# Kernel tuning notes

Measured on AMD Instinct MI355X. Metric: run time of the kernel, lower is better.

## Reference

```python
import jax, jax.numpy as jnp
import numpy as np

HIDDEN = 1024
N_HEADS = 16
HEAD_DIM = HIDDEN // N_HEADS


def setup_inputs() -> dict:
    key = jax.random.key(0)
    ks = jax.random.split(key, 9)
    s = 1.0 / np.sqrt(HIDDEN)
    d = {"hidden_states": jax.random.normal(ks[0], (2, 2048, HIDDEN), dtype=jnp.float32)}
    for i, name in enumerate(["q", "k", "v", "o"]):
        d[f"W{name}"] = jax.random.uniform(ks[1 + 2 * i], (HIDDEN, HIDDEN), minval=-s, maxval=s, dtype=jnp.float32)
        d[f"b{name}"] = jax.random.uniform(ks[2 + 2 * i], (HIDDEN,), minval=-s, maxval=s, dtype=jnp.float32)
    return d


def reference(hidden_states, Wq, bq, Wk, bk, Wv, bv, Wo, bo):
    B, L, _ = hidden_states.shape

    def shape(x):  # (B, L, H*D) -> (B, H, L, D)
        return x.reshape(B, L, N_HEADS, HEAD_DIM).transpose(0, 2, 1, 3)

    q = shape(hidden_states @ Wq.T + bq)
    k = shape(hidden_states @ Wk.T + bk)
    v = shape(hidden_states @ Wv.T + bv)
    scores = jnp.einsum("bhqd,bhkd->bhqk", q, k) / jnp.sqrt(jnp.float32(HEAD_DIM))
    attn = jax.nn.softmax(scores, axis=-1)
    ctx = jnp.einsum("bhqk,bhkd->bhqd", attn, v)
    ctx = ctx.transpose(0, 2, 1, 3).reshape(B, L, HIDDEN)
    return ctx @ Wo.T + bo
```

## Files before the change

### kernel.cpp

```cpp
#include <hip/hip_runtime.h>
#include <hip/hip_bf16.h>
#include <stdint.h>

typedef __bf16 bf16_t;
typedef __bf16 bf16x8 __attribute__((ext_vector_type(8)));
typedef __bf16 bf16x4 __attribute__((ext_vector_type(4)));
typedef float  f32x4  __attribute__((ext_vector_type(4)));
typedef float  f32x16 __attribute__((ext_vector_type(16)));

__device__ __forceinline__ f32x4 mfma16(bf16x8 a, bf16x8 b, f32x4 c) {
    return __builtin_amdgcn_mfma_f32_16x16x32_bf16(a, b, c, 0, 0, 0);
}
__device__ __forceinline__ f32x16 mfma32(bf16x8 a, bf16x8 b, f32x16 c) {
    return __builtin_amdgcn_mfma_f32_32x32x16_bf16(a, b, c, 0, 0, 0);
}
__device__ __forceinline__ void gload16(const void* g, void* l) {
    __builtin_amdgcn_global_load_lds(
        (const __attribute__((address_space(1))) unsigned int*)g,
        (__attribute__((address_space(3))) unsigned int*)l, 16, 0, 0);
}
__device__ __forceinline__ unsigned cvtpk(float lo, float hi_) {
    unsigned r;
    asm("v_cvt_pk_bf16_f32 %0, %1, %2" : "=v"(r) : "v"(lo), "v"(hi_));
    return r;
}
__device__ __forceinline__ float fexp2(float x) {
    return __builtin_amdgcn_exp2f(x);
}

__global__ __launch_bounds__(256) void split_all(const float* __restrict__ X,
                                                 const float* __restrict__ w0, const float* __restrict__ w1,
                                                 const float* __restrict__ w2, const float* __restrict__ w3,
                                                 bf16_t* __restrict__ xh,
                                                 bf16_t* __restrict__ h0, bf16_t* __restrict__ h1,
                                                 bf16_t* __restrict__ h2, bf16_t* __restrict__ h3) {
    int blk = blockIdx.x;
    const float* in;
    bf16_t* hi;
    int i;
    if (blk < 2048) {
        in = X; hi = xh;
        i = blk * 256 + threadIdx.x;
    } else {
        int s = (blk - 2048) >> 9;
        in = (s == 0) ? w0 : (s == 1) ? w1 : (s == 2) ? w2 : w3;
        hi = (s == 0) ? h0 : (s == 1) ? h1 : (s == 2) ? h2 : h3;
        i = ((blk - 2048) & 511) * 256 + threadIdx.x;
    }
    int row = i >> 7;
    int di = (i & ~3) | ((i & 3) ^ ((row >> 1) & 3));
    const float4* in4 = reinterpret_cast<const float4*>(in);
    float4 v0 = in4[2 * i], v1 = in4[2 * i + 1];
    float vv[8] = {v0.x, v0.y, v0.z, v0.w, v1.x, v1.y, v1.z, v1.w};
    bf16x8 h;
#pragma unroll
    for (int j = 0; j < 8; ++j) h[j] = (bf16_t)vv[j];
    reinterpret_cast<bf16x8*>(hi)[di] = h;
}

__global__ __launch_bounds__(512) void gemm_qkv(const bf16_t* __restrict__ Xhi,
                                                const bf16_t* __restrict__ Wqh,
                                                const bf16_t* __restrict__ Wkh,
                                                const bf16_t* __restrict__ Wvh,
                                                const float* __restrict__ bq, const float* __restrict__ bk,
                                                const float* __restrict__ bv,
                                                bf16_t* __restrict__ Qb, bf16_t* __restrict__ Kb,
                                                bf16_t* __restrict__ Vt) {
    __shared__ alignas(16) bf16_t ldsA[2][128 * 32];
    __shared__ alignas(16) bf16_t ldsB[2][128 * 32];
    const int tid = threadIdx.x, wave = tid >> 6, lane = tid & 63;
    const int g = lane >> 4, cc = lane & 15;
    const int bx = blockIdx.x, which = bx >> 3;
    const bf16_t* Bh = (which == 0) ? Wqh : (which == 1) ? Wkh : Wvh;
    const float* bias = (which == 0) ? bq : (which == 1) ? bk : bv;
    const float scale = (which == 0) ? 0.125f * 1.4426950408889634f : 1.0f;
    const int mBase = blockIdx.y * 128, nB = (bx & 7) * 128;
    const int wm = wave >> 2, wn = wave & 3;

    f32x4 zero = {0.f, 0.f, 0.f, 0.f};
    f32x4 acc[4][2];
#pragma unroll
    for (int mi = 0; mi < 4; ++mi)
#pragma unroll
        for (int ni = 0; ni < 2; ++ni) acc[mi][ni] = zero;

    auto stage = [&](int k0, int buf) {
#pragma unroll
        for (int i = 0; i < 2; ++i) {
            int c = wave + 8 * i;
            int tile = c >> 3, sub = c & 7;
            int row = sub * 16 + (lane >> 2);
            int colE = (lane & 3) * 8;
            const bf16_t* src = (tile == 0) ? Xhi + (size_t)(mBase + row) * 1024 + k0 + colE
                                            : Bh + (size_t)(nB + row) * 1024 + k0 + colE;
            bf16_t* dst = (tile == 0) ? ldsA[buf] : ldsB[buf];
            gload16(src, (char*)dst + sub * 1024);
        }
    };

    stage(0, 0);
    for (int t = 0; t < 32; ++t) {
        const int buf = t & 1;
        asm volatile("s_waitcnt vmcnt(0)" ::: "memory");
        __builtin_amdgcn_s_barrier();
        __builtin_amdgcn_sched_barrier(0);
        if (t < 31) stage((t + 1) * 32, buf ^ 1);
        {
            bf16x8 af[4], bf_[2];
#pragma unroll
            for (int mi = 0; mi < 4; ++mi) {
                int ra = wm * 64 + mi * 16 + cc;
                af[mi] = *reinterpret_cast<const bf16x8*>(
                    (const char*)ldsA[buf] + ra * 64 + ((g ^ ((ra >> 1) & 3)) * 16));
            }
#pragma unroll
            for (int ni = 0; ni < 2; ++ni) {
                int rb = wn * 32 + ni * 16 + cc;
                bf_[ni] = *reinterpret_cast<const bf16x8*>(
                    (const char*)ldsB[buf] + rb * 64 + ((g ^ ((rb >> 1) & 3)) * 16));
            }
#pragma unroll
            for (int mi = 0; mi < 4; ++mi)
#pragma unroll
                for (int ni = 0; ni < 2; ++ni)
                    acc[mi][ni] = mfma16(af[mi], bf_[ni], acc[mi][ni]);
        }
    }

#pragma unroll
    for (int mi = 0; mi < 4; ++mi)
#pragma unroll
        for (int ni = 0; ni < 2; ++ni)
#pragma unroll
            for (int r = 0; r < 4; ++r) {
                int row = mBase + wm * 64 + mi * 16 + g * 4 + r;
                int colL = nB + wn * 32 + ni * 16 + cc;
                float v = (acc[mi][ni][r] + bias[colL]) * scale;
                int b = row >> 11, tok = row & 2047, h = colL >> 6, d = colL & 63;
                if (which == 2) {
                    int kt = tok >> 6, key = tok & 63;
                    size_t o = (((size_t)(b * 16 + h) * 32 + kt) * 4096)
                             + d * 64 + ((((key >> 3) ^ (d & 7)) << 3) | (key & 7));
                    Vt[o] = (bf16_t)v;
                } else {
                    int dd = (which == 1) ? ((((d >> 3) ^ (tok & 7)) << 3) | (d & 7)) : d;
                    bf16_t* out = (which == 0) ? Qb : Kb;
                    out[((size_t)(b * 16 + h) * 2048 + tok) * 64 + dd] = (bf16_t)v;
                }
            }
}

__global__ __launch_bounds__(512) void gemm_o(const bf16_t* __restrict__ Ahi,
                                              const bf16_t* __restrict__ Bhi,
                                              const float* __restrict__ bias,
                                              float* __restrict__ outF) {
    __shared__ alignas(16) bf16_t ldsA[2][64 * 32];
    __shared__ alignas(16) bf16_t ldsB[2][128 * 32];
    const int tid = threadIdx.x, wave = tid >> 6, lane = tid & 63;
    const int g = lane >> 4, cc = lane & 15;
    const int mBase = blockIdx.y * 64, nBase = blockIdx.x * 128;
    const int wm = wave >> 2, wn = wave & 3;

    f32x4 zero = {0.f, 0.f, 0.f, 0.f};
    f32x4 acc[2][2];
#pragma unroll
    for (int mi = 0; mi < 2; ++mi)
#pragma unroll
        for (int ni = 0; ni < 2; ++ni) acc[mi][ni] = zero;

    auto stage = [&](int k0, int buf) {
#pragma unroll
        for (int i = 0; i < 2; ++i) {
            int c = wave + 8 * i;
            if (c >= 12) continue;
            const bf16_t* srcb;
            bf16_t* dst;
            int sub, rbase;
            if (c < 4) { srcb = Ahi; dst = ldsA[buf]; sub = c;     rbase = mBase; }
            else       { srcb = Bhi; dst = ldsB[buf]; sub = c - 4; rbase = nBase; }
            int row = sub * 16 + (lane >> 2);
            int colE = (lane & 3) * 8;
            gload16(srcb + (size_t)(rbase + row) * 1024 + k0 + colE, (char*)dst + sub * 1024);
        }
    };

    stage(0, 0);
    for (int t = 0; t < 32; ++t) {
        const int buf = t & 1;
        asm volatile("s_waitcnt vmcnt(0)" ::: "memory");
        __builtin_amdgcn_s_barrier();
        __builtin_amdgcn_sched_barrier(0);
        if (t < 31) stage((t + 1) * 32, buf ^ 1);
        {
            bf16x8 af[2], bf_[2];
#pragma unroll
            for (int mi = 0; mi < 2; ++mi) {
                int ra = wm * 32 + mi * 16 + cc;
                af[mi] = *reinterpret_cast<const bf16x8*>(
                    (const char*)ldsA[buf] + ra * 64 + ((g ^ ((ra >> 1) & 3)) * 16));
            }
#pragma unroll
            for (int ni = 0; ni < 2; ++ni) {
                int rb = wn * 32 + ni * 16 + cc;
                bf_[ni] = *reinterpret_cast<const bf16x8*>(
                    (const char*)ldsB[buf] + rb * 64 + ((g ^ ((rb >> 1) & 3)) * 16));
            }
#pragma unroll
            for (int mi = 0; mi < 2; ++mi)
#pragma unroll
                for (int ni = 0; ni < 2; ++ni)
                    acc[mi][ni] = mfma16(af[mi], bf_[ni], acc[mi][ni]);
        }
    }

#pragma unroll
    for (int mi = 0; mi < 2; ++mi)
#pragma unroll
        for (int ni = 0; ni < 2; ++ni)
#pragma unroll
            for (int r = 0; r < 4; ++r) {
                int row = mBase + wm * 32 + mi * 16 + g * 4 + r;
                int col = nBase + wn * 32 + ni * 16 + cc;
                outF[(size_t)row * 1024 + col] = acc[mi][ni][r] + bias[col];
            }
}

__global__ __launch_bounds__(512, 4) void attn_kernel(const bf16_t* __restrict__ Qb,
                                                      const bf16_t* __restrict__ Kb_p,
                                                      const bf16_t* __restrict__ Vt_p,
                                                      bf16_t* __restrict__ ctxHi) {
    __shared__ alignas(16) bf16_t SB[2][16384];

    const int lid = blockIdx.x;
    const int xcd = lid & 7, slot = lid >> 3;
    const int bh = xcd * 4 + (slot & 3);
    const int qt = slot >> 2;

    const int tid = threadIdx.x, w = tid >> 6, l = tid & 63;
    const int ql = l & 31, hi = l >> 5;
    const int wq = w & 3;
    const int par = w >> 2;
    const size_t kbase = (size_t)bh * 2048 * 64;
    const unsigned rsw = (unsigned)(ql & 7) << 4;

    bf16x8 qf[4];
    {
        const bf16_t* qp = Qb + kbase + (size_t)(qt * 128 + wq * 32 + ql) * 64 + hi * 8;
#pragma unroll
        for (int c = 0; c < 4; ++c) qf[c] = *reinterpret_cast<const bf16x8*>(qp + c * 16);
    }
    bf16x8 ones;
#pragma unroll
    for (int j = 0; j < 8; ++j) ones[j] = (bf16_t)1.0f;

    f32x16 O0{}, O1{}, Lacc{};

    auto stage = [&](int r) {
        int buf = r & 1;
        const bf16_t* ks = Kb_p + kbase + (size_t)(2 * r) * 4096;
        const bf16_t* vs = Vt_p + ((size_t)bh * 32 + 2 * r) * 4096;
        char* kd = (char*)&SB[buf][0];
        char* vd = (char*)&SB[buf][8192];
        gload16(ks + (size_t)tid * 8,        kd + tid * 16);
        gload16(ks + (size_t)tid * 8 + 4096, kd + tid * 16 + 8192);
        gload16(vs + (size_t)tid * 8,        vd + tid * 16);
        gload16(vs + (size_t)tid * 8 + 4096, vd + tid * 16 + 8192);
    };

    stage(0);

    for (int r = 0; r < 16; ++r) {
        const int buf = r & 1;
        asm volatile("s_waitcnt vmcnt(0)" ::: "memory");
        __builtin_amdgcn_s_barrier();
        __builtin_amdgcn_sched_barrier(0);
        if (r < 15) stage(r + 1);

        const char* kb = (const char*)&SB[buf][par * 4096];
        const char* vb = (const char*)&SB[buf][8192 + par * 4096];

        f32x16 S0{}, S1{};
        __builtin_amdgcn_s_setprio(1);
#pragma unroll
        for (int c = 0; c < 4; ++c) {
            unsigned col = ((unsigned)(c * 32 + hi * 16)) ^ rsw;
            bf16x8 k0 = *reinterpret_cast<const bf16x8*>(kb + (unsigned)ql * 128 + col);
            bf16x8 k1 = *reinterpret_cast<const bf16x8*>(kb + (unsigned)(32 + ql) * 128 + col);
            S0 = mfma32(k0, qf[c], S0);
            S1 = mfma32(k1, qf[c], S1);
        }
        __builtin_amdgcn_s_setprio(0);

#pragma unroll
        for (int r2 = 0; r2 < 16; ++r2) {
            S0[r2] = fexp2(S0[r2]);
            S1[r2] = fexp2(S1[r2]);
        }

        union U { unsigned u[4]; bf16x8 v; };
        bf16x8 PB[4];
#define MKFRAG(DST, SS, M8)                                                       \
        {                                                                         \
            unsigned c0 = cvtpk(SS[M8 + 0], SS[M8 + 1]);                          \
            unsigned c1 = cvtpk(SS[M8 + 2], SS[M8 + 3]);                          \
            unsigned c2 = cvtpk(SS[M8 + 4], SS[M8 + 5]);                          \
            unsigned c3 = cvtpk(SS[M8 + 6], SS[M8 + 7]);                          \
            unsigned y0 = hi ? c0 : c2;                                           \
            unsigned y1 = hi ? c1 : c3;                                           \
            unsigned z0 = (unsigned)__shfl_xor((int)y0, 32);                      \
            unsigned z1 = (unsigned)__shfl_xor((int)y1, 32);                      \
            U uu;                                                                 \
            uu.u[0] = hi ? z0 : c0;                                               \
            uu.u[1] = hi ? z1 : c1;                                               \
            uu.u[2] = hi ? c2 : z0;                                               \
            uu.u[3] = hi ? c3 : z1;                                               \
            DST = uu.v;                                                           \
        }
        MKFRAG(PB[0], S0, 0)
        MKFRAG(PB[1], S0, 8)
        MKFRAG(PB[2], S1, 0)
        MKFRAG(PB[3], S1, 8)
#undef MKFRAG

        __builtin_amdgcn_s_setprio(1);
#pragma unroll
        for (int ks = 0; ks < 4; ++ks) {
            unsigned col = ((unsigned)(ks * 32 + hi * 16)) ^ rsw;
            bf16x8 v0 = *reinterpret_cast<const bf16x8*>(vb + (unsigned)ql * 128 + col);
            bf16x8 v1 = *reinterpret_cast<const bf16x8*>(vb + (unsigned)(32 + ql) * 128 + col);
            O0 = mfma32(v0, PB[ks], O0);
            O1 = mfma32(v1, PB[ks], O1);
            Lacc = mfma32(ones, PB[ks], Lacc);
        }
        __builtin_amdgcn_s_setprio(0);
    }

    __builtin_amdgcn_s_barrier();

    float lsum = Lacc[0];
    float* mbuf = (float*)&SB[0][0];
    if (par == 1) {
        float* p = mbuf + (size_t)(wq * 64 + l) * 33;
        p[0] = lsum;
#pragma unroll
        for (int r2 = 0; r2 < 16; ++r2) { p[1 + r2] = O0[r2]; p[17 + r2] = O1[r2]; }
    }
    __syncthreads();
    if (par == 1) return;

    {
        const float* p = mbuf + (size_t)(wq * 64 + l) * 33;
        lsum += p[0];
#pragma unroll
        for (int r2 = 0; r2 < 16; ++r2) {
            O0[r2] += p[1 + r2];
            O1[r2] += p[17 + r2];
        }
    }

    const int b = bh >> 4, h = bh & 15;
    const int ltok = qt * 128 + wq * 32 + ql;
    const float inv = 1.0f / lsum;
    bf16_t* baseH = ctxHi + ((size_t)(b * 2048 + ltok)) * 1024 + h * 64;
    const int rsw4 = (ql >> 1) & 3;
#define WRITE4(OT, RQ, DT)                                                      \
    {                                                                           \
        int d0 = (RQ ^ rsw4) * 8 + 4 * hi + 32 * DT;                            \
        bf16x4 vh;                                                              \
        _Pragma("unroll")                                                       \
        for (int i = 0; i < 4; ++i) {                                           \
            float v = OT[4 * RQ + i] * inv;                                     \
            vh[i] = (bf16_t)v;                                                  \
        }                                                                       \
        *reinterpret_cast<bf16x4*>(baseH + d0) = vh;                            \
    }
    WRITE4(O0, 0, 0) WRITE4(O0, 1, 0) WRITE4(O0, 2, 0) WRITE4(O0, 3, 0)
    WRITE4(O1, 0, 1) WRITE4(O1, 1, 1) WRITE4(O1, 2, 1) WRITE4(O1, 3, 1)
#undef WRITE4
}

extern "C" void kernel_launch(void* const* d_in, const int* in_sizes, int n_in,
                              void* d_out, int out_size, void* d_ws, size_t ws_size,
                              hipStream_t stream) {
    const float* X  = (const float*)d_in[0];
    const float* Wq = (const float*)d_in[1];
    const float* bq = (const float*)d_in[2];
    const float* Wk = (const float*)d_in[3];
    const float* bk = (const float*)d_in[4];
    const float* Wv = (const float*)d_in[5];
    const float* bv = (const float*)d_in[6];
    const float* Wo = (const float*)d_in[7];
    const float* bo = (const float*)d_in[8];

    const size_t MB = 1024 * 1024;
    char* ws = (char*)d_ws;
    bf16_t* Xhi = (bf16_t*)(ws);
    bf16_t* Wqh = (bf16_t*)(ws + 8 * MB);
    bf16_t* Wkh = (bf16_t*)(ws + 10 * MB);
    bf16_t* Wvh = (bf16_t*)(ws + 12 * MB);
    bf16_t* Woh = (bf16_t*)(ws + 14 * MB);
    bf16_t* Qb  = (bf16_t*)(ws + 24 * MB);
    bf16_t* Kb  = (bf16_t*)(ws + 32 * MB);
    bf16_t* Vt  = (bf16_t*)(ws + 40 * MB);
    bf16_t* Chi = (bf16_t*)(ws + 48 * MB);

    split_all<<<4096, 256, 0, stream>>>(X, Wq, Wk, Wv, Wo,
                                        Xhi, Wqh, Wkh, Wvh, Woh);

    dim3 qkvGrid(24, 32);
    gemm_qkv<<<qkvGrid, 512, 0, stream>>>(Xhi, Wqh, Wkh, Wvh,
                                          bq, bk, bv, Qb, Kb, Vt);

    attn_kernel<<<512, 512, 0, stream>>>(Qb, Kb, Vt, Chi);

    dim3 oGrid(8, 64);
    gemm_o<<<oGrid, 512, 0, stream>>>(Chi, Woh, bo, (float*)d_out);
}
```

Baseline: 112.4 us.

## Triple-buffer GEMM loads and drop key-split reduction in attention

Both GEMMs move from double to triple-buffered LDS staging with a partial vmcnt wait, so the load for tile t+2 is in flight while tile t is computed. The output GEMM goes to 256 threads, with each wave covering all 64 rows and a 32-column slice. The attention kernel drops its two-way key split across wave groups and the LDS reduction at the end; it now runs 256 threads per block that walk all 32 key tiles, with occupancy hint 5. This removes the reduction and a barrier but halves the per-block parallelism and doubles the serial key loop.

```diff
diff --git a/kernel.cpp b/kernel.cpp
--- a/kernel.cpp
+++ b/kernel.cpp
@@ -66,8 +66,8 @@
                                                 const float* __restrict__ bv,
                                                 bf16_t* __restrict__ Qb, bf16_t* __restrict__ Kb,
                                                 bf16_t* __restrict__ Vt) {
-    __shared__ alignas(16) bf16_t ldsA[2][128 * 32];
-    __shared__ alignas(16) bf16_t ldsB[2][128 * 32];
+    __shared__ alignas(16) bf16_t ldsA[3][128 * 32];
+    __shared__ alignas(16) bf16_t ldsB[3][128 * 32];
     const int tid = threadIdx.x, wave = tid >> 6, lane = tid & 63;
     const int g = lane >> 4, cc = lane & 15;
     const int bx = blockIdx.x, which = bx >> 3;
@@ -99,25 +99,30 @@
     };
 
     stage(0, 0);
+    stage(32, 1);
+    int cur = 0;
     for (int t = 0; t < 32; ++t) {
-        const int buf = t & 1;
-        asm volatile("s_waitcnt vmcnt(0)" ::: "memory");
+        if (t < 31) asm volatile("s_waitcnt vmcnt(2)" ::: "memory");
+        else        asm volatile("s_waitcnt vmcnt(0)" ::: "memory");
         __builtin_amdgcn_s_barrier();
         __builtin_amdgcn_sched_barrier(0);
-        if (t < 31) stage((t + 1) * 32, buf ^ 1);
+        if (t + 2 < 32) {
+            int stg = cur + 2; if (stg >= 3) stg -= 3;
+            stage((t + 2) * 32, stg);
+        }
         {
             bf16x8 af[4], bf_[2];
 #pragma unroll
             for (int mi = 0; mi < 4; ++mi) {
                 int ra = wm * 64 + mi * 16 + cc;
                 af[mi] = *reinterpret_cast<const bf16x8*>(
-                    (const char*)ldsA[buf] + ra * 64 + ((g ^ ((ra >> 1) & 3)) * 16));
+                    (const char*)ldsA[cur] + ra * 64 + ((g ^ ((ra >> 1) & 3)) * 16));
             }
 #pragma unroll
             for (int ni = 0; ni < 2; ++ni) {
                 int rb = wn * 32 + ni * 16 + cc;
                 bf_[ni] = *reinterpret_cast<const bf16x8*>(
-                    (const char*)ldsB[buf] + rb * 64 + ((g ^ ((rb >> 1) & 3)) * 16));
+                    (const char*)ldsB[cur] + rb * 64 + ((g ^ ((rb >> 1) & 3)) * 16));
             }
 #pragma unroll
             for (int mi = 0; mi < 4; ++mi)
@@ -125,6 +130,7 @@
                 for (int ni = 0; ni < 2; ++ni)
                     acc[mi][ni] = mfma16(af[mi], bf_[ni], acc[mi][ni]);
         }
+        cur = (cur == 2) ? 0 : cur + 1;
     }
 
 #pragma unroll
@@ -150,29 +156,27 @@
             }
 }
 
-__global__ __launch_bounds__(512) void gemm_o(const bf16_t* __restrict__ Ahi,
+__global__ __launch_bounds__(256) void gemm_o(const bf16_t* __restrict__ Ahi,
                                               const bf16_t* __restrict__ Bhi,
                                               const float* __restrict__ bias,
                                               float* __restrict__ outF) {
-    __shared__ alignas(16) bf16_t ldsA[2][64 * 32];
-    __shared__ alignas(16) bf16_t ldsB[2][128 * 32];
+    __shared__ alignas(16) bf16_t ldsA[3][64 * 32];
+    __shared__ alignas(16) bf16_t ldsB[3][128 * 32];
     const int tid = threadIdx.x, wave = tid >> 6, lane = tid & 63;
     const int g = lane >> 4, cc = lane & 15;
     const int mBase = blockIdx.y * 64, nBase = blockIdx.x * 128;
-    const int wm = wave >> 2, wn = wave & 3;
 
     f32x4 zero = {0.f, 0.f, 0.f, 0.f};
-    f32x4 acc[2][2];
-#pragma unroll
-    for (int mi = 0; mi < 2; ++mi)
+    f32x4 acc[4][2];
+#pragma unroll
+    for (int mi = 0; mi < 4; ++mi)
 #pragma unroll
         for (int ni = 0; ni < 2; ++ni) acc[mi][ni] = zero;
 
     auto stage = [&](int k0, int buf) {
 #pragma unroll
-        for (int i = 0; i < 2; ++i) {
-            int c = wave + 8 * i;
-            if (c >= 12) continue;
+        for (int i = 0; i < 3; ++i) {
+            int c = wave + 4 * i;
             const bf16_t* srcb;
             bf16_t* dst;
             int sub, rbase;
@@ -185,51 +189,57 @@
     };
 
     stage(0, 0);
+    stage(32, 1);
+    int cur = 0;
     for (int t = 0; t < 32; ++t) {
-        const int buf = t & 1;
-        asm volatile("s_waitcnt vmcnt(0)" ::: "memory");
+        if (t < 31) asm volatile("s_waitcnt vmcnt(3)" ::: "memory");
+        else        asm volatile("s_waitcnt vmcnt(0)" ::: "memory");
         __builtin_amdgcn_s_barrier();
         __builtin_amdgcn_sched_barrier(0);
-        if (t < 31) stage((t + 1) * 32, buf ^ 1);
+        if (t + 2 < 32) {
+            int stg = cur + 2; if (stg >= 3) stg -= 3;
+            stage((t + 2) * 32, stg);
+        }
         {
-            bf16x8 af[2], bf_[2];
-#pragma unroll
-            for (int mi = 0; mi < 2; ++mi) {
-                int ra = wm * 32 + mi * 16 + cc;
+            bf16x8 af[4], bf_[2];
+#pragma unroll
+            for (int mi = 0; mi < 4; ++mi) {
+                int ra = mi * 16 + cc;
                 af[mi] = *reinterpret_cast<const bf16x8*>(
-                    (const char*)ldsA[buf] + ra * 64 + ((g ^ ((ra >> 1) & 3)) * 16));
+                    (const char*)ldsA[cur] + ra * 64 + ((g ^ ((ra >> 1) & 3)) * 16));
             }
 #pragma unroll
             for (int ni = 0; ni < 2; ++ni) {
-                int rb = wn * 32 + ni * 16 + cc;
+                int rb = wave * 32 + ni * 16 + cc;
                 bf_[ni] = *reinterpret_cast<const bf16x8*>(
-                    (const char*)ldsB[buf] + rb * 64 + ((g ^ ((rb >> 1) & 3)) * 16));
-            }
-#pragma unroll
-            for (int mi = 0; mi < 2; ++mi)
+                    (const char*)ldsB[cur] + rb * 64 + ((g ^ ((rb >> 1) & 3)) * 16));
+            }
+#pragma unroll
+            for (int mi = 0; mi < 4; ++mi)
 #pragma unroll
                 for (int ni = 0; ni < 2; ++ni)
                     acc[mi][ni] = mfma16(af[mi], bf_[ni], acc[mi][ni]);
         }
-    }
-
-#pragma unroll
-    for (int mi = 0; mi < 2; ++mi)
+        cur = (cur == 2) ? 0 : cur + 1;
+    }
+
+#pragma unroll
+    for (int mi = 0; mi < 4; ++mi)
 #pragma unroll
         for (int ni = 0; ni < 2; ++ni)
 #pragma unroll
             for (int r = 0; r < 4; ++r) {
-                int row = mBase + wm * 32 + mi * 16 + g * 4 + r;
-                int col = nBase + wn * 32 + ni * 16 + cc;
+                int row = mBase + mi * 16 + g * 4 + r;
+                int col = nBase + wave * 32 + ni * 16 + cc;
                 outF[(size_t)row * 1024 + col] = acc[mi][ni][r] + bias[col];
             }
 }
 
-__global__ __launch_bounds__(512, 4) void attn_kernel(const bf16_t* __restrict__ Qb,
+__global__ __launch_bounds__(256, 5) void attn_kernel(const bf16_t* __restrict__ Qb,
                                                       const bf16_t* __restrict__ Kb_p,
                                                       const bf16_t* __restrict__ Vt_p,
                                                       bf16_t* __restrict__ ctxHi) {
-    __shared__ alignas(16) bf16_t SB[2][16384];
+    __shared__ alignas(16) bf16_t SB[2][8192];
 
     const int lid = blockIdx.x;
     const int xcd = lid & 7, slot = lid >> 3;
@@ -238,14 +248,12 @@
 
     const int tid = threadIdx.x, w = tid >> 6, l = tid & 63;
     const int ql = l & 31, hi = l >> 5;
-    const int wq = w & 3;
-    const int par = w >> 2;
     const size_t kbase = (size_t)bh * 2048 * 64;
     const unsigned rsw = (unsigned)(ql & 7) << 4;
 
     bf16x8 qf[4];
     {
-        const bf16_t* qp = Qb + kbase + (size_t)(qt * 128 + wq * 32 + ql) * 64 + hi * 8;
+        const bf16_t* qp = Qb + kbase + (size_t)(qt * 128 + w * 32 + ql) * 64 + hi * 8;
 #pragma unroll
         for (int c = 0; c < 4; ++c) qf[c] = *reinterpret_cast<const bf16x8*>(qp + c * 16);
     }
@@ -257,27 +265,27 @@
 
     auto stage = [&](int r) {
         int buf = r & 1;
-        const bf16_t* ks = Kb_p + kbase + (size_t)(2 * r) * 4096;
-        const bf16_t* vs = Vt_p + ((size_t)bh * 32 + 2 * r) * 4096;
+        const bf16_t* ks = Kb_p + kbase + (size_t)r * 4096;
+        const bf16_t* vs = Vt_p + ((size_t)bh * 32 + r) * 4096;
         char* kd = (char*)&SB[buf][0];
-        char* vd = (char*)&SB[buf][8192];
+        char* vd = (char*)&SB[buf][4096];
         gload16(ks + (size_t)tid * 8,        kd + tid * 16);
-        gload16(ks + (size_t)tid * 8 + 4096, kd + tid * 16 + 8192);
+        gload16(ks + (size_t)tid * 8 + 2048, kd + tid * 16 + 4096);
         gload16(vs + (size_t)tid * 8,        vd + tid * 16);
-        gload16(vs + (size_t)tid * 8 + 4096, vd + tid * 16 + 8192);
+        gload16(vs + (size_t)tid * 8 + 2048, vd + tid * 16 + 4096);
     };
 
     stage(0);
 
-    for (int r = 0; r < 16; ++r) {
+    for (int r = 0; r < 32; ++r) {
         const int buf = r & 1;
         asm volatile("s_waitcnt vmcnt(0)" ::: "memory");
         __builtin_amdgcn_s_barrier();
         __builtin_amdgcn_sched_barrier(0);
-        if (r < 15) stage(r + 1);
-
-        const char* kb = (const char*)&SB[buf][par * 4096];
-        const char* vb = (const char*)&SB[buf][8192 + par * 4096];
+        if (r < 31) stage(r + 1);
+
+        const char* kb = (const char*)&SB[buf][0];
+        const char* vb = (const char*)&SB[buf][4096];
 
         f32x16 S0{}, S1{};
         __builtin_amdgcn_s_setprio(1);
@@ -335,31 +343,9 @@
         __builtin_amdgcn_s_setprio(0);
     }
 
-    __builtin_amdgcn_s_barrier();
-
-    float lsum = Lacc[0];
-    float* mbuf = (float*)&SB[0][0];
-    if (par == 1) {
-        float* p = mbuf + (size_t)(wq * 64 + l) * 33;
-        p[0] = lsum;
-#pragma unroll
-        for (int r2 = 0; r2 < 16; ++r2) { p[1 + r2] = O0[r2]; p[17 + r2] = O1[r2]; }
-    }
-    __syncthreads();
-    if (par == 1) return;
-
-    {
-        const float* p = mbuf + (size_t)(wq * 64 + l) * 33;
-        lsum += p[0];
-#pragma unroll
-        for (int r2 = 0; r2 < 16; ++r2) {
-            O0[r2] += p[1 + r2];
-            O1[r2] += p[17 + r2];
-        }
-    }
-
+    const float lsum = Lacc[0];
     const int b = bh >> 4, h = bh & 15;
-    const int ltok = qt * 128 + wq * 32 + ql;
+    const int ltok = qt * 128 + w * 32 + ql;
     const float inv = 1.0f / lsum;
     bf16_t* baseH = ctxHi + ((size_t)(b * 2048 + ltok)) * 1024 + h * 64;
     const int rsw4 = (ql >> 1) & 3;
@@ -411,8 +397,8 @@
     gemm_qkv<<<qkvGrid, 512, 0, stream>>>(Xhi, Wqh, Wkh, Wvh,
                                           bq, bk, bv, Qb, Kb, Vt);
 
-    attn_kernel<<<512, 512, 0, stream>>>(Qb, Kb, Vt, Chi);
+    attn_kernel<<<512, 256, 0, stream>>>(Qb, Kb, Vt, Chi);
 
     dim3 oGrid(8, 64);
-    gemm_o<<<oGrid, 512, 0, stream>>>(Chi, Woh, bo, (float*)d_out);
-}
+    gemm_o<<<oGrid, 256, 0, stream>>>(Chi, Woh, bo, (float*)d_out);
+}
```

Measured after the change: 156.2 us. +39.0%, slower.
